# Kernel optimization log

Measured on AMD Instinct MI355X. Metric: run time of the kernel, lower is better.

Reference implementation:

```python
import jax, jax.numpy as jnp
import numpy as np

B, T, O = 32, 2048, 18            # batch, triples per graph, hardcoded object count
DIN1, H, DOUT = 1500, 512, 512    # net1 input dim is hardcoded 1500 in the source

def _kaiming(key, fan_in, fan_out):
    return jax.random.normal(key, (fan_in, fan_out), jnp.float32) * np.sqrt(2.0 / fan_in)

def setup_inputs() -> dict:
    key = jax.random.key(0)
    ks = jax.random.split(key, 8)
    trip = jax.random.normal(ks[0], (B, T, DIN1), jnp.float32)
    index = jax.random.randint(ks[1], (B, T, 2), 0, O)
    rel_lens = jax.random.randint(ks[2], (B,), 0, T)
    # net1: 1500 -> H -> 2H+Dout (ReLU after every layer incl. last)
    w1a = _kaiming(ks[3], DIN1, H); b1a = jnp.zeros((H,), jnp.float32)
    w1b = _kaiming(ks[4], H, 2 * H + DOUT); b1b = jnp.zeros((2 * H + DOUT,), jnp.float32)
    # net2: H -> H -> Dout (ReLU after every layer incl. last)
    w2a = _kaiming(ks[5], H, H); b2a = jnp.zeros((H,), jnp.float32)
    w2b = _kaiming(ks[6], H, DOUT); b2b = jnp.zeros((DOUT,), jnp.float32)
    return dict(trip=trip, index=index, rel_lens=rel_lens,
                w1a=w1a, b1a=b1a, w1b=w1b, b1b=b1b,
                w2a=w2a, b2a=b2a, w2b=w2b, b2b=b2b)

def reference(trip, index, rel_lens, w1a, b1a, w1b, b1b, w2a, b2a, w2b, b2b):
    # net1 MLP over all triples: [B,T,1500] -> [B,T,2H+Dout]
    h = jax.nn.relu(trip @ w1a + b1a)
    new_t = jax.nn.relu(h @ w1b + b1b)
    s_vecs = new_t[..., :H]              # [B,T,H] subject
    p_vecs = new_t[..., H:H + DOUT]      # [B,T,Dout] predicate (returned as-is)
    o_vecs = new_t[..., H + DOUT:]       # [B,T,H] object
    # mask out triples beyond rel_lens[i]
    mask = (jnp.arange(T)[None, :] < rel_lens[:, None]).astype(new_t.dtype)  # [B,T]
    oh_s = jax.nn.one_hot(index[..., 0], O, dtype=new_t.dtype) * mask[..., None]  # [B,T,O]
    oh_o = jax.nn.one_hot(index[..., 1], O, dtype=new_t.dtype) * mask[..., None]
    # per-batch scatter_add pooling into the O=18 object slots
    contrib = (jnp.einsum('bto,bth->boh', oh_s, s_vecs)
               + jnp.einsum('bto,bth->boh', oh_o, o_vecs))  # [B,O,H]
    # original code never resets pooled_obj_vecs inside the batch loop ->
    # accumulation is CUMULATIVE over batch items
    pooled = jnp.cumsum(contrib, axis=0)  # [B,O,H]
    # net2 MLP on each cumulative pool
    h2 = jax.nn.relu(pooled @ w2a + b2a)
    new_obj = jax.nn.relu(h2 @ w2b + b2b)  # [B,O,Dout]
    return new_obj, p_vecs
```

## Files before the change

kernel.cpp:

```cpp
#include <hip/hip_runtime.h>
#include <hip/hip_bf16.h>

#define NBATCH 32
#define NTIME  2048
#define NOBJ   18
#define KIN    1500
#define NH     512
#define NTOT   1536
#define NM     65536

typedef __attribute__((ext_vector_type(4))) float f32x4;
typedef __attribute__((ext_vector_type(8))) short s16x8;
typedef __attribute__((ext_vector_type(4))) short s16x4;

static __device__ __forceinline__ short f2bf(float f) {
  union { float f; unsigned u; } v; v.f = f;
  unsigned r = v.u + 0x7fffu + ((v.u >> 16) & 1u);
  return (short)(r >> 16);
}

static __device__ __forceinline__ void gload_lds16(const short* g, short* l) {
  __builtin_amdgcn_global_load_lds(
      (const __attribute__((address_space(1))) unsigned int*)(g),
      (__attribute__((address_space(3))) unsigned int*)(l), 16, 0, 0);
}

__global__ void k_prep(const float* __restrict__ src, short* __restrict__ dst,
                       int K, int Nsrc, int nkt, int total) {
  int i = blockIdx.x * 256 + threadIdx.x;
  if (i >= total) return;
  int chunk = i >> 14, off = i & 16383;
  int row = off >> 6, kcp = off & 63;
  int kc = kcp ^ ((row & 7) << 3);
  int cb = chunk / nkt, kt = chunk - cb * nkt;
  int n = cb * 256 + row, k = kt * 64 + kc;
  dst[i] = (k < K) ? f2bf(src[(size_t)k * Nsrc + n]) : (short)0;
}

__global__ void k_zero(float* __restrict__ p, int n) {
  int i = blockIdx.x * 256 + threadIdx.x;
  if (i < n) p[i] = 0.f;
}

__launch_bounds__(512, 2)
__global__ void k_gemm1(const float* __restrict__ A, const short* __restrict__ Bc,
                        const float* __restrict__ bias, short* __restrict__ Hc) {
  __shared__ short lA[2][64 * 64];
  __shared__ short lB[2][256 * 64];
  const int g = blockIdx.x;
  const int lid = (g & 7) * 256 + (g >> 3);
  const int rb = lid >> 1, cb = lid & 1;
  const int m0 = rb * 64, n0 = cb * 256;
  const int tid = threadIdx.x;
  const int lane = tid & 63, w = tid >> 6;
  const int wr = w >> 2, wc = w & 3;
  const int rlane = lane & 15, ksel = (lane >> 4) * 8;
  const int arow = tid >> 4;
  const int akq  = (tid & 15) * 4;
  const short* bchunk = Bc + (size_t)(cb * 24) * 16384;

  f32x4 acc[2][4] = {};
  float4 av[2];

  auto issue_stage = [&](int nb, int kt) {
    const int kbase = kt * 64;
    const bool fullq = (kt < 23) | (akq <= 24);
#pragma unroll
    for (int ri = 0; ri < 2; ++ri) {
      const float* p = A + (size_t)(m0 + arow + ri * 32) * KIN + kbase + akq;
      av[ri] = fullq ? *(const float4*)p : make_float4(0.f, 0.f, 0.f, 0.f);
    }
    const short* src = bchunk + (size_t)kt * 16384 + tid * 8;
#pragma unroll
    for (int i = 0; i < 4; ++i)
      gload_lds16(src + i * 4096, &lB[nb][tid * 8 + i * 4096]);
  };
  auto write_stage = [&](int nb) {
#pragma unroll
    for (int ri = 0; ri < 2; ++ri) {
      int row = arow + ri * 32;
      s16x4 h4;
      h4[0] = f2bf(av[ri].x); h4[1] = f2bf(av[ri].y);
      h4[2] = f2bf(av[ri].z); h4[3] = f2bf(av[ri].w);
      *(s16x4*)&lA[nb][row * 64 + (akq ^ ((row & 7) << 3))] = h4;
    }
  };
  auto compute = [&](int cu) {
#pragma unroll
    for (int j = 0; j < 2; ++j) {
      int k0 = j * 32 + ksel;
      s16x8 af[2], bfr[4];
#pragma unroll
      for (int m = 0; m < 2; ++m) {
        int row = wr * 32 + m * 16 + rlane;
        af[m] = *(const s16x8*)&lA[cu][row * 64 + (k0 ^ ((row & 7) << 3))];
      }
#pragma unroll
      for (int n = 0; n < 4; ++n) {
        int row = wc * 64 + n * 16 + rlane;
        bfr[n] = *(const s16x8*)&lB[cu][row * 64 + (k0 ^ ((row & 7) << 3))];
      }
#pragma unroll
      for (int m = 0; m < 2; ++m)
#pragma unroll
        for (int n = 0; n < 4; ++n)
          acc[m][n] = __builtin_amdgcn_mfma_f32_16x16x32_bf16(af[m], bfr[n], acc[m][n], 0, 0, 0);
    }
  };

  issue_stage(0, 0);
  write_stage(0);
  asm volatile("s_waitcnt vmcnt(0)" ::: "memory");
  __syncthreads();
  for (int kt = 0; kt < 24; ++kt) {
    const int cu = kt & 1;
    if (kt < 23) issue_stage(cu ^ 1, kt + 1);
    compute(cu);
    if (kt < 23) {
      write_stage(cu ^ 1);
      asm volatile("s_waitcnt vmcnt(0)" ::: "memory");
      __syncthreads();
    }
  }

#pragma unroll
  for (int n = 0; n < 4; ++n) {
    int c = n0 + wc * 64 + n * 16 + rlane;
    float bv = bias[c];
#pragma unroll
    for (int m = 0; m < 2; ++m) {
      int rbase = m0 + wr * 32 + m * 16 + ((lane >> 4) << 2);
#pragma unroll
      for (int q = 0; q < 4; ++q) {
        int r = rbase + q;
        float v = acc[m][n][q] + bv;
        v = v > 0.f ? v : 0.f;
        Hc[(size_t)(((r >> 7) * 8 + (c >> 6)) * 8192) + (r & 127) * 64 +
           ((c & 63) ^ ((r & 7) << 3))] = f2bf(v);
      }
    }
  }
}

__launch_bounds__(512, 2)
__global__ void k_gemm2(const short* __restrict__ Ac, const short* __restrict__ Bc,
                        const float* __restrict__ bias, const int* __restrict__ index,
                        const int* __restrict__ rel_lens,
                        float* __restrict__ contrib, float* __restrict__ out) {
  __shared__ short lA[2][64 * 64];
  __shared__ short lB[2][256 * 64];
  const int g = blockIdx.x;
  const int lid = (g & 7) * 768 + (g >> 3);
  const int rb = lid / 6, cb = lid - rb * 6;
  const int m0 = rb * 64, n0 = cb * 256;
  const int region = n0 >> 9;
  const int b = m0 >> 11;
  const int rel = rel_lens[b];
  if (region != 1 && (m0 & 2047) >= rel) return;

  const int tid = threadIdx.x;
  const int lane = tid & 63, w = tid >> 6;
  const int wr = w >> 2, wc = w & 3;
  const int rlane = lane & 15, ksel = (lane >> 4) * 8;
  const short* achunk = Ac + (size_t)((m0 >> 7) * 8) * 8192 + (m0 & 127) * 64;
  const short* bchunk = Bc + (size_t)(cb * 8) * 16384;

  f32x4 acc[2][4] = {};

  auto issue_stage = [&](int nb, int kt) {
    gload_lds16(achunk + (size_t)kt * 8192 + tid * 8, &lA[nb][tid * 8]);
    const short* src = bchunk + (size_t)kt * 16384 + tid * 8;
#pragma unroll
    for (int i = 0; i < 4; ++i)
      gload_lds16(src + i * 4096, &lB[nb][tid * 8 + i * 4096]);
  };
  auto compute = [&](int cu) {
#pragma unroll
    for (int j = 0; j < 2; ++j) {
      int k0 = j * 32 + ksel;
      s16x8 af[2], bfr[4];
#pragma unroll
      for (int m = 0; m < 2; ++m) {
        int row = wr * 32 + m * 16 + rlane;
        af[m] = *(const s16x8*)&lA[cu][row * 64 + (k0 ^ ((row & 7) << 3))];
      }
#pragma unroll
      for (int n = 0; n < 4; ++n) {
        int row = wc * 64 + n * 16 + rlane;
        bfr[n] = *(const s16x8*)&lB[cu][row * 64 + (k0 ^ ((row & 7) << 3))];
      }
#pragma unroll
      for (int m = 0; m < 2; ++m)
#pragma unroll
        for (int n = 0; n < 4; ++n)
          acc[m][n] = __builtin_amdgcn_mfma_f32_16x16x32_bf16(af[m], bfr[n], acc[m][n], 0, 0, 0);
    }
  };

  issue_stage(0, 0);
  asm volatile("s_waitcnt vmcnt(0)" ::: "memory");
  __syncthreads();
  for (int kt = 0; kt < 8; ++kt) {
    const int cu = kt & 1;
    if (kt < 7) issue_stage(cu ^ 1, kt + 1);
    compute(cu);
    if (kt < 7) {
      asm volatile("s_waitcnt vmcnt(0)" ::: "memory");
      __syncthreads();
    }
  }

  float bv[4]; int cg[4];
#pragma unroll
  for (int n = 0; n < 4; ++n) { cg[n] = n0 + wc * 64 + n * 16 + rlane; bv[n] = bias[cg[n]]; }

  if (region == 1) {
    float* po = out + (size_t)NBATCH * NOBJ * NH;
#pragma unroll
    for (int m = 0; m < 2; ++m) {
      int rbase = m0 + wr * 32 + m * 16 + ((lane >> 4) << 2);
#pragma unroll
      for (int q = 0; q < 4; ++q) {
#pragma unroll
        for (int n = 0; n < 4; ++n) {
          float v = acc[m][n][q] + bv[n];
          v = v > 0.f ? v : 0.f;
          po[(size_t)(rbase + q) * NH + (cg[n] & 511)] = v;
        }
      }
    }
  } else {
    const int sel = region >> 1;
#pragma unroll
    for (int m = 0; m < 2; ++m) {
      int rbase = m0 + wr * 32 + m * 16 + ((lane >> 4) << 2);
#pragma unroll
      for (int q = 0; q < 4; ++q) {
        int r = rbase + q;
        if ((r & 2047) < rel) {
          int idx = index[2 * r + sel];
          float* dst = contrib + ((b * NOBJ + idx) << 9);
#pragma unroll
          for (int n = 0; n < 4; ++n) {
            float v = acc[m][n][q] + bv[n];
            v = v > 0.f ? v : 0.f;
            atomicAdd(dst + (cg[n] & 511), v);
          }
        }
      }
    }
  }
}

__global__ void k_cumsum(const float* __restrict__ contrib, float* __restrict__ pooled) {
  int i = blockIdx.x * 256 + threadIdx.x;
  if (i >= NOBJ * NH) return;
  float a = 0.f;
#pragma unroll
  for (int b = 0; b < NBATCH; ++b) {
    a += contrib[b * (NOBJ * NH) + i];
    pooled[b * (NOBJ * NH) + i] = a;
  }
}

__global__ void k_mlp2(const float* __restrict__ pooled,
                       const float* __restrict__ w2a, const float* __restrict__ b2a,
                       const float* __restrict__ w2b, const float* __restrict__ b2b,
                       float* __restrict__ out) {
  __shared__ float pr[NH];
  __shared__ float hr[NH];
  int row = blockIdx.x;
  int tid = threadIdx.x;
  pr[tid]       = pooled[(size_t)row * NH + tid];
  pr[tid + 256] = pooled[(size_t)row * NH + tid + 256];
  __syncthreads();
  {
    float a0 = 0.f, a1 = 0.f, b0 = 0.f, b1 = 0.f;
    for (int k = 0; k < NH; k += 2) {
      float p0 = pr[k], p1 = pr[k + 1];
      a0 += p0 * w2a[(size_t)k * NH + tid];
      b0 += p0 * w2a[(size_t)k * NH + tid + 256];
      a1 += p1 * w2a[(size_t)(k + 1) * NH + tid];
      b1 += p1 * w2a[(size_t)(k + 1) * NH + tid + 256];
    }
    float s0 = a0 + a1 + b2a[tid], s1 = b0 + b1 + b2a[tid + 256];
    hr[tid]       = s0 > 0.f ? s0 : 0.f;
    hr[tid + 256] = s1 > 0.f ? s1 : 0.f;
  }
  __syncthreads();
  {
    float a0 = 0.f, a1 = 0.f, b0 = 0.f, b1 = 0.f;
    for (int k = 0; k < NH; k += 2) {
      float h0 = hr[k], h1 = hr[k + 1];
      a0 += h0 * w2b[(size_t)k * NH + tid];
      b0 += h0 * w2b[(size_t)k * NH + tid + 256];
      a1 += h1 * w2b[(size_t)(k + 1) * NH + tid];
      b1 += h1 * w2b[(size_t)(k + 1) * NH + tid + 256];
    }
    float s0 = a0 + a1 + b2b[tid], s1 = b0 + b1 + b2b[tid + 256];
    out[(size_t)row * NH + tid]       = s0 > 0.f ? s0 : 0.f;
    out[(size_t)row * NH + tid + 256] = s1 > 0.f ? s1 : 0.f;
  }
}

extern "C" void kernel_launch(void* const* d_in, const int* in_sizes, int n_in,
                              void* d_out, int out_size, void* d_ws, size_t ws_size,
                              hipStream_t stream) {
  const float* trip     = (const float*)d_in[0];
  const int*   index    = (const int*)d_in[1];
  const int*   rel_lens = (const int*)d_in[2];
  const float* w1a      = (const float*)d_in[3];
  const float* b1a      = (const float*)d_in[4];
  const float* w1b      = (const float*)d_in[5];
  const float* b1b      = (const float*)d_in[6];
  const float* w2a      = (const float*)d_in[7];
  const float* b2a      = (const float*)d_in[8];
  const float* w2b      = (const float*)d_in[9];
  const float* b2b      = (const float*)d_in[10];
  float* out = (float*)d_out;

  char* ws = (char*)d_ws;
  short* wt1a    = (short*)(ws);
  short* wt1b    = (short*)(ws + 1572864);
  short* hbuf    = (short*)(ws + 3145728);
  float* contrib = (float*)(ws + 70254592);
  float* pooled  = contrib + NBATCH * NOBJ * NH;

  k_zero<<<1152, 256, 0, stream>>>(contrib, NBATCH * NOBJ * NH);
  k_prep<<<3072, 256, 0, stream>>>(w1a, wt1a, KIN, NH, 24, NH * 1536);
  k_prep<<<3072, 256, 0, stream>>>(w1b, wt1b, NH, NTOT, 8, NTOT * NH);
  k_gemm1<<<2048, 512, 0, stream>>>(trip, wt1a, b1a, hbuf);
  k_gemm2<<<6144, 512, 0, stream>>>(hbuf, wt1b, b1b, index, rel_lens, contrib, out);
  k_cumsum<<<36, 256, 0, stream>>>(contrib, pooled);
  k_mlp2<<<576, 256, 0, stream>>>(pooled, w2a, b2a, w2b, b2b, out);
}
```

Before: 475.7 us.

## Fuse both net1 GEMMs into one kernel keeping hidden activations in LDS

After: 1.607 ms. 3.38x slower.

```diff
diff --git a/kernel.cpp b/kernel.cpp
--- a/kernel.cpp
+++ b/kernel.cpp
@@ -24,6 +24,10 @@
       (const __attribute__((address_space(1))) unsigned int*)(g),
       (__attribute__((address_space(3))) unsigned int*)(l), 16, 0, 0);
 }
+
+#define FENCE() asm volatile("" ::: "memory")
+#define BAR()   do { FENCE(); __builtin_amdgcn_s_barrier(); FENCE(); } while (0)
+#define LGKM0() asm volatile("s_waitcnt lgkmcnt(0)" ::: "memory")
 
 __global__ void k_prep(const float* __restrict__ src, short* __restrict__ dst,
                        int K, int Nsrc, int nkt, int total) {
@@ -43,208 +47,209 @@
 }
 
 __launch_bounds__(512, 2)
-__global__ void k_gemm1(const float* __restrict__ A, const short* __restrict__ Bc,
-                        const float* __restrict__ bias, short* __restrict__ Hc) {
-  __shared__ short lA[2][64 * 64];
+__global__ void k_fused(const float* __restrict__ A, const short* __restrict__ B1c,
+                        const float* __restrict__ b1a, const short* __restrict__ B2c,
+                        const float* __restrict__ b1b, const int* __restrict__ index,
+                        const int* __restrict__ rel_lens,
+                        float* __restrict__ contrib, float* __restrict__ out) {
+  __shared__ short hS[64 * 512];
+  __shared__ short lA[64 * 128];
   __shared__ short lB[2][256 * 64];
   const int g = blockIdx.x;
-  const int lid = (g & 7) * 256 + (g >> 3);
-  const int rb = lid >> 1, cb = lid & 1;
-  const int m0 = rb * 64, n0 = cb * 256;
+  const int lid = (g & 7) * 128 + (g >> 3);
+  const int m0 = lid * 64;
+  const int b = m0 >> 11;
+  const int rel = rel_lens[b];
   const int tid = threadIdx.x;
   const int lane = tid & 63, w = tid >> 6;
   const int wr = w >> 2, wc = w & 3;
   const int rlane = lane & 15, ksel = (lane >> 4) * 8;
-  const int arow = tid >> 4;
-  const int akq  = (tid & 15) * 4;
-  const short* bchunk = Bc + (size_t)(cb * 24) * 16384;
-
-  f32x4 acc[2][4] = {};
-  float4 av[2];
-
-  auto issue_stage = [&](int nb, int kt) {
-    const int kbase = kt * 64;
-    const bool fullq = (kt < 23) | (akq <= 24);
-#pragma unroll
-    for (int ri = 0; ri < 2; ++ri) {
-      const float* p = A + (size_t)(m0 + arow + ri * 32) * KIN + kbase + akq;
-      av[ri] = fullq ? *(const float4*)p : make_float4(0.f, 0.f, 0.f, 0.f);
-    }
-    const short* src = bchunk + (size_t)kt * 16384 + tid * 8;
+  const int arow = tid >> 3;
+  const int aseg = tid & 7;
+
+  f32x4 acc1[2][2][4] = {};
+  float4 av[4];
+  s16x8 af[2], bfr[4];
+
+  auto issueA = [&](int u) {
+#pragma unroll
+    for (int i = 0; i < 4; ++i) {
+      int k = u * 128 + aseg * 16 + i * 4;
+      const float* p = A + (size_t)(m0 + arow) * KIN + k;
+      av[i] = (k + 4 <= KIN) ? *(const float4*)p : make_float4(0.f, 0.f, 0.f, 0.f);
+    }
+  };
+  auto writeA = [&]() {
+#pragma unroll
+    for (int i = 0; i < 4; ++i) {
+      int c = aseg * 16 + i * 4;
+      s16x4 h4;
+      h4[0] = f2bf(av[i].x); h4[1] = f2bf(av[i].y);
+      h4[2] = f2bf(av[i].z); h4[3] = f2bf(av[i].w);
+      *(s16x4*)&lA[arow * 128 + (c & 64) + ((c & 63) ^ ((arow & 7) << 3))] = h4;
+    }
+  };
+  auto issueB1 = [&](int nb, int cb, int kt) {
+    const short* src = B1c + (size_t)(cb * 24 + kt) * 16384 + tid * 8;
 #pragma unroll
     for (int i = 0; i < 4; ++i)
       gload_lds16(src + i * 4096, &lB[nb][tid * 8 + i * 4096]);
   };
-  auto write_stage = [&](int nb) {
-#pragma unroll
-    for (int ri = 0; ri < 2; ++ri) {
-      int row = arow + ri * 32;
-      s16x4 h4;
-      h4[0] = f2bf(av[ri].x); h4[1] = f2bf(av[ri].y);
-      h4[2] = f2bf(av[ri].z); h4[3] = f2bf(av[ri].w);
-      *(s16x4*)&lA[nb][row * 64 + (akq ^ ((row & 7) << 3))] = h4;
-    }
-  };
-  auto compute = [&](int cu) {
-#pragma unroll
-    for (int j = 0; j < 2; ++j) {
-      int k0 = j * 32 + ksel;
-      s16x8 af[2], bfr[4];
-#pragma unroll
-      for (int m = 0; m < 2; ++m) {
-        int row = wr * 32 + m * 16 + rlane;
-        af[m] = *(const s16x8*)&lA[cu][row * 64 + (k0 ^ ((row & 7) << 3))];
-      }
-#pragma unroll
-      for (int n = 0; n < 4; ++n) {
-        int row = wc * 64 + n * 16 + rlane;
-        bfr[n] = *(const s16x8*)&lB[cu][row * 64 + (k0 ^ ((row & 7) << 3))];
-      }
-#pragma unroll
-      for (int m = 0; m < 2; ++m)
-#pragma unroll
-        for (int n = 0; n < 4; ++n)
-          acc[m][n] = __builtin_amdgcn_mfma_f32_16x16x32_bf16(af[m], bfr[n], acc[m][n], 0, 0, 0);
-    }
-  };
-
-  issue_stage(0, 0);
-  write_stage(0);
-  asm volatile("s_waitcnt vmcnt(0)" ::: "memory");
-  __syncthreads();
-  for (int kt = 0; kt < 24; ++kt) {
-    const int cu = kt & 1;
-    if (kt < 23) issue_stage(cu ^ 1, kt + 1);
-    compute(cu);
-    if (kt < 23) {
-      write_stage(cu ^ 1);
-      asm volatile("s_waitcnt vmcnt(0)" ::: "memory");
-      __syncthreads();
-    }
-  }
-
-#pragma unroll
-  for (int n = 0; n < 4; ++n) {
-    int c = n0 + wc * 64 + n * 16 + rlane;
-    float bv = bias[c];
-#pragma unroll
-    for (int m = 0; m < 2; ++m) {
-      int rbase = m0 + wr * 32 + m * 16 + ((lane >> 4) << 2);
-#pragma unroll
-      for (int q = 0; q < 4; ++q) {
-        int r = rbase + q;
-        float v = acc[m][n][q] + bv;
-        v = v > 0.f ? v : 0.f;
-        Hc[(size_t)(((r >> 7) * 8 + (c >> 6)) * 8192) + (r & 127) * 64 +
-           ((c & 63) ^ ((r & 7) << 3))] = f2bf(v);
-      }
-    }
-  }
-}
-
-__launch_bounds__(512, 2)
-__global__ void k_gemm2(const short* __restrict__ Ac, const short* __restrict__ Bc,
-                        const float* __restrict__ bias, const int* __restrict__ index,
-                        const int* __restrict__ rel_lens,
-                        float* __restrict__ contrib, float* __restrict__ out) {
-  __shared__ short lA[2][64 * 64];
-  __shared__ short lB[2][256 * 64];
-  const int g = blockIdx.x;
-  const int lid = (g & 7) * 768 + (g >> 3);
-  const int rb = lid / 6, cb = lid - rb * 6;
-  const int m0 = rb * 64, n0 = cb * 256;
-  const int region = n0 >> 9;
-  const int b = m0 >> 11;
-  const int rel = rel_lens[b];
-  if (region != 1 && (m0 & 2047) >= rel) return;
-
-  const int tid = threadIdx.x;
-  const int lane = tid & 63, w = tid >> 6;
-  const int wr = w >> 2, wc = w & 3;
-  const int rlane = lane & 15, ksel = (lane >> 4) * 8;
-  const short* achunk = Ac + (size_t)((m0 >> 7) * 8) * 8192 + (m0 & 127) * 64;
-  const short* bchunk = Bc + (size_t)(cb * 8) * 16384;
-
-  f32x4 acc[2][4] = {};
-
-  auto issue_stage = [&](int nb, int kt) {
-    gload_lds16(achunk + (size_t)kt * 8192 + tid * 8, &lA[nb][tid * 8]);
-    const short* src = bchunk + (size_t)kt * 16384 + tid * 8;
+  auto issueB2 = [&](int nb, int p, int kt) {
+    const short* src = B2c + (size_t)(p * 8 + kt) * 16384 + tid * 8;
 #pragma unroll
     for (int i = 0; i < 4; ++i)
       gload_lds16(src + i * 4096, &lB[nb][tid * 8 + i * 4096]);
   };
-  auto compute = [&](int cu) {
+
+  issueA(0);
+  issueB1(0, 0, 0);
+  asm volatile("s_waitcnt vmcnt(0)" ::: "memory");
+  writeA();
+  LGKM0();
+  BAR();
+
+#pragma unroll 1
+  for (int s = 0; s < 48; ++s) {
+    const int u = s >> 2, half = (s >> 1) & 1, sub = s & 1;
+    const int cu = s & 1;
+    if (s < 47) {
+      const int s1 = s + 1;
+      issueB1(cu ^ 1, (s1 >> 1) & 1, (s1 >> 2) * 2 + (s1 & 1));
+    }
+    const bool aIss = ((s & 3) == 1) && (u < 11);
+    if (aIss) issueA(u + 1);
 #pragma unroll
     for (int j = 0; j < 2; ++j) {
       int k0 = j * 32 + ksel;
-      s16x8 af[2], bfr[4];
 #pragma unroll
       for (int m = 0; m < 2; ++m) {
         int row = wr * 32 + m * 16 + rlane;
-        af[m] = *(const s16x8*)&lA[cu][row * 64 + (k0 ^ ((row & 7) << 3))];
-      }
-#pragma unroll
-      for (int n = 0; n < 4; ++n) {
-        int row = wc * 64 + n * 16 + rlane;
-        bfr[n] = *(const s16x8*)&lB[cu][row * 64 + (k0 ^ ((row & 7) << 3))];
+        af[m] = *(const s16x8*)&lA[row * 128 + sub * 64 + (k0 ^ ((row & 7) << 3))];
+      }
+#pragma unroll
+      for (int nn = 0; nn < 4; ++nn) {
+        int row = wc * 64 + nn * 16 + rlane;
+        bfr[nn] = *(const s16x8*)&lB[cu][row * 64 + (k0 ^ ((row & 7) << 3))];
       }
 #pragma unroll
       for (int m = 0; m < 2; ++m)
 #pragma unroll
-        for (int n = 0; n < 4; ++n)
-          acc[m][n] = __builtin_amdgcn_mfma_f32_16x16x32_bf16(af[m], bfr[n], acc[m][n], 0, 0, 0);
-    }
-  };
-
-  issue_stage(0, 0);
-  asm volatile("s_waitcnt vmcnt(0)" ::: "memory");
-  __syncthreads();
-  for (int kt = 0; kt < 8; ++kt) {
-    const int cu = kt & 1;
-    if (kt < 7) issue_stage(cu ^ 1, kt + 1);
-    compute(cu);
-    if (kt < 7) {
-      asm volatile("s_waitcnt vmcnt(0)" ::: "memory");
-      __syncthreads();
-    }
-  }
-
-  float bv[4]; int cg[4];
-#pragma unroll
-  for (int n = 0; n < 4; ++n) { cg[n] = n0 + wc * 64 + n * 16 + rlane; bv[n] = bias[cg[n]]; }
-
-  if (region == 1) {
-    float* po = out + (size_t)NBATCH * NOBJ * NH;
-#pragma unroll
-    for (int m = 0; m < 2; ++m) {
-      int rbase = m0 + wr * 32 + m * 16 + ((lane >> 4) << 2);
-#pragma unroll
-      for (int q = 0; q < 4; ++q) {
-#pragma unroll
-        for (int n = 0; n < 4; ++n) {
-          float v = acc[m][n][q] + bv[n];
+        for (int nn = 0; nn < 4; ++nn)
+          acc1[half][m][nn] = __builtin_amdgcn_mfma_f32_16x16x32_bf16(
+              af[m], bfr[nn], acc1[half][m][nn], 0, 0, 0);
+    }
+    if (s < 47) {
+      if (aIss) { asm volatile("s_waitcnt vmcnt(4)" ::: "memory"); }
+      else      { asm volatile("s_waitcnt vmcnt(0)" ::: "memory"); }
+      BAR();
+      if (((s & 3) == 3) && (u < 11)) {
+        writeA();
+        LGKM0();
+        BAR();
+      }
+    }
+  }
+
+#pragma unroll
+  for (int half = 0; half < 2; ++half)
+#pragma unroll
+    for (int nn = 0; nn < 4; ++nn) {
+      int c = half * 256 + wc * 64 + nn * 16 + rlane;
+      float bv = b1a[c];
+      int csw = (c & ~63);
+#pragma unroll
+      for (int m = 0; m < 2; ++m) {
+        int lr0 = wr * 32 + m * 16 + ((lane >> 4) << 2);
+#pragma unroll
+        for (int q = 0; q < 4; ++q) {
+          int lr = lr0 + q;
+          float v = acc1[half][m][nn][q] + bv;
           v = v > 0.f ? v : 0.f;
-          po[(size_t)(rbase + q) * NH + (cg[n] & 511)] = v;
-        }
-      }
-    }
-  } else {
-    const int sel = region >> 1;
-#pragma unroll
-    for (int m = 0; m < 2; ++m) {
-      int rbase = m0 + wr * 32 + m * 16 + ((lane >> 4) << 2);
-#pragma unroll
-      for (int q = 0; q < 4; ++q) {
-        int r = rbase + q;
-        if ((r & 2047) < rel) {
-          int idx = index[2 * r + sel];
-          float* dst = contrib + ((b * NOBJ + idx) << 9);
-#pragma unroll
-          for (int n = 0; n < 4; ++n) {
-            float v = acc[m][n][q] + bv[n];
+          hS[lr * 512 + csw + ((c & 63) ^ ((lr & 7) << 3))] = f2bf(v);
+        }
+      }
+    }
+  LGKM0();
+  BAR();
+
+#pragma unroll 1
+  for (int p = 0; p < 6; ++p) {
+    const int region = p >> 1;
+    if (region != 1 && (m0 & 2047) >= rel) continue;
+
+    f32x4 acc2[2][4] = {};
+    issueB2(0, p, 0);
+    asm volatile("s_waitcnt vmcnt(0)" ::: "memory");
+    BAR();
+#pragma unroll 1
+    for (int kt = 0; kt < 8; ++kt) {
+      const int cu = kt & 1;
+      if (kt < 7) issueB2(cu ^ 1, p, kt + 1);
+#pragma unroll
+      for (int j = 0; j < 2; ++j) {
+        int k0 = j * 32 + ksel;
+#pragma unroll
+        for (int m = 0; m < 2; ++m) {
+          int row = wr * 32 + m * 16 + rlane;
+          af[m] = *(const s16x8*)&hS[row * 512 + kt * 64 + (k0 ^ ((row & 7) << 3))];
+        }
+#pragma unroll
+        for (int nn = 0; nn < 4; ++nn) {
+          int row = wc * 64 + nn * 16 + rlane;
+          bfr[nn] = *(const s16x8*)&lB[cu][row * 64 + (k0 ^ ((row & 7) << 3))];
+        }
+#pragma unroll
+        for (int m = 0; m < 2; ++m)
+#pragma unroll
+          for (int nn = 0; nn < 4; ++nn)
+            acc2[m][nn] = __builtin_amdgcn_mfma_f32_16x16x32_bf16(
+                af[m], bfr[nn], acc2[m][nn], 0, 0, 0);
+      }
+      if (kt < 7) {
+        asm volatile("s_waitcnt vmcnt(0)" ::: "memory");
+        BAR();
+      }
+    }
+
+    float bv[4]; int cg[4];
+#pragma unroll
+    for (int nn = 0; nn < 4; ++nn) {
+      cg[nn] = p * 256 + wc * 64 + nn * 16 + rlane;
+      bv[nn] = b1b[cg[nn]];
+    }
+    if (region == 1) {
+      float* po = out + (size_t)NBATCH * NOBJ * NH;
+#pragma unroll
+      for (int m = 0; m < 2; ++m) {
+        int rbase = m0 + wr * 32 + m * 16 + ((lane >> 4) << 2);
+#pragma unroll
+        for (int q = 0; q < 4; ++q) {
+#pragma unroll
+          for (int nn = 0; nn < 4; ++nn) {
+            float v = acc2[m][nn][q] + bv[nn];
             v = v > 0.f ? v : 0.f;
-            atomicAdd(dst + (cg[n] & 511), v);
+            po[(size_t)(rbase + q) * NH + (cg[nn] & 511)] = v;
+          }
+        }
+      }
+    } else {
+      const int sel = region >> 1;
+#pragma unroll
+      for (int m = 0; m < 2; ++m) {
+        int rbase = m0 + wr * 32 + m * 16 + ((lane >> 4) << 2);
+#pragma unroll
+        for (int q = 0; q < 4; ++q) {
+          int r = rbase + q;
+          if ((r & 2047) < rel) {
+            int idx = index[2 * r + sel];
+            float* dst = contrib + ((b * NOBJ + idx) << 9);
+#pragma unroll
+            for (int nn = 0; nn < 4; ++nn) {
+              float v = acc2[m][nn][q] + bv[nn];
+              v = v > 0.f ? v : 0.f;
+              atomicAdd(dst + (cg[nn] & 511), v);
+            }
           }
         }
       }
@@ -322,15 +327,14 @@
   char* ws = (char*)d_ws;
   short* wt1a    = (short*)(ws);
   short* wt1b    = (short*)(ws + 1572864);
-  short* hbuf    = (short*)(ws + 3145728);
-  float* contrib = (float*)(ws + 70254592);
+  float* contrib = (float*)(ws + 3145728);
   float* pooled  = contrib + NBATCH * NOBJ * NH;
 
   k_zero<<<1152, 256, 0, stream>>>(contrib, NBATCH * NOBJ * NH);
   k_prep<<<3072, 256, 0, stream>>>(w1a, wt1a, KIN, NH, 24, NH * 1536);
   k_prep<<<3072, 256, 0, stream>>>(w1b, wt1b, NH, NTOT, 8, NTOT * NH);
-  k_gemm1<<<2048, 512, 0, stream>>>(trip, wt1a, b1a, hbuf);
-  k_gemm2<<<6144, 512, 0, stream>>>(hbuf, wt1b, b1b, index, rel_lens, contrib, out);
+  k_fused<<<1024, 512, 0, stream>>>(trip, wt1a, b1a, wt1b, b1b, index, rel_lens,
+                                    contrib, out);
   k_cumsum<<<36, 256, 0, stream>>>(contrib, pooled);
   k_mlp2<<<576, 256, 0, stream>>>(pooled, w2a, b2a, w2b, b2b, out);
 }
```

## Enlarge gemm1 M tile to 128 rows with single-buffered A in LDS

Applied to the files above, without the earlier changes.

New measurement: 501.5 us. 1.05x slower.

```diff
diff --git a/kernel.cpp b/kernel.cpp
--- a/kernel.cpp
+++ b/kernel.cpp
@@ -24,6 +24,10 @@
       (const __attribute__((address_space(1))) unsigned int*)(g),
       (__attribute__((address_space(3))) unsigned int*)(l), 16, 0, 0);
 }
+
+#define FENCE() asm volatile("" ::: "memory")
+#define BAR()   do { FENCE(); __builtin_amdgcn_s_barrier(); FENCE(); } while (0)
+#define LGKM0() asm volatile("s_waitcnt lgkmcnt(0)" ::: "memory")
 
 __global__ void k_prep(const float* __restrict__ src, short* __restrict__ dst,
                        int K, int Nsrc, int nkt, int total) {
@@ -45,95 +49,103 @@
 __launch_bounds__(512, 2)
 __global__ void k_gemm1(const float* __restrict__ A, const short* __restrict__ Bc,
                         const float* __restrict__ bias, short* __restrict__ Hc) {
-  __shared__ short lA[2][64 * 64];
+  __shared__ short lA[128 * 64];
   __shared__ short lB[2][256 * 64];
   const int g = blockIdx.x;
-  const int lid = (g & 7) * 256 + (g >> 3);
+  const int lid = (g & 7) * 128 + (g >> 3);
   const int rb = lid >> 1, cb = lid & 1;
-  const int m0 = rb * 64, n0 = cb * 256;
+  const int m0 = rb * 128, n0 = cb * 256;
   const int tid = threadIdx.x;
   const int lane = tid & 63, w = tid >> 6;
   const int wr = w >> 2, wc = w & 3;
   const int rlane = lane & 15, ksel = (lane >> 4) * 8;
-  const int arow = tid >> 4;
-  const int akq  = (tid & 15) * 4;
+  const int arow = tid >> 2;
+  const int akq  = (tid & 3) * 16;
   const short* bchunk = Bc + (size_t)(cb * 24) * 16384;
 
-  f32x4 acc[2][4] = {};
-  float4 av[2];
-
-  auto issue_stage = [&](int nb, int kt) {
-    const int kbase = kt * 64;
-    const bool fullq = (kt < 23) | (akq <= 24);
-#pragma unroll
-    for (int ri = 0; ri < 2; ++ri) {
-      const float* p = A + (size_t)(m0 + arow + ri * 32) * KIN + kbase + akq;
-      av[ri] = fullq ? *(const float4*)p : make_float4(0.f, 0.f, 0.f, 0.f);
-    }
+  f32x4 acc[4][4] = {};
+  float4 av[4];
+  s16x8 af[4], bfr[4];
+
+  auto issueAregs = [&](int kt) {
+    const int kbase = kt * 64 + akq;
+#pragma unroll
+    for (int i = 0; i < 4; ++i) {
+      int k = kbase + i * 4;
+      const float* p = A + (size_t)(m0 + arow) * KIN + k;
+      av[i] = (k + 4 <= KIN) ? *(const float4*)p : make_float4(0.f, 0.f, 0.f, 0.f);
+    }
+  };
+  auto writeA = [&]() {
+#pragma unroll
+    for (int i = 0; i < 4; ++i) {
+      int c = akq + i * 4;
+      s16x4 h4;
+      h4[0] = f2bf(av[i].x); h4[1] = f2bf(av[i].y);
+      h4[2] = f2bf(av[i].z); h4[3] = f2bf(av[i].w);
+      *(s16x4*)&lA[arow * 64 + (c ^ ((arow & 7) << 3))] = h4;
+    }
+  };
+  auto issueB = [&](int nb, int kt) {
     const short* src = bchunk + (size_t)kt * 16384 + tid * 8;
 #pragma unroll
     for (int i = 0; i < 4; ++i)
       gload_lds16(src + i * 4096, &lB[nb][tid * 8 + i * 4096]);
   };
-  auto write_stage = [&](int nb) {
-#pragma unroll
-    for (int ri = 0; ri < 2; ++ri) {
-      int row = arow + ri * 32;
-      s16x4 h4;
-      h4[0] = f2bf(av[ri].x); h4[1] = f2bf(av[ri].y);
-      h4[2] = f2bf(av[ri].z); h4[3] = f2bf(av[ri].w);
-      *(s16x4*)&lA[nb][row * 64 + (akq ^ ((row & 7) << 3))] = h4;
-    }
-  };
   auto compute = [&](int cu) {
 #pragma unroll
     for (int j = 0; j < 2; ++j) {
       int k0 = j * 32 + ksel;
-      s16x8 af[2], bfr[4];
-#pragma unroll
-      for (int m = 0; m < 2; ++m) {
-        int row = wr * 32 + m * 16 + rlane;
-        af[m] = *(const s16x8*)&lA[cu][row * 64 + (k0 ^ ((row & 7) << 3))];
-      }
-#pragma unroll
-      for (int n = 0; n < 4; ++n) {
-        int row = wc * 64 + n * 16 + rlane;
-        bfr[n] = *(const s16x8*)&lB[cu][row * 64 + (k0 ^ ((row & 7) << 3))];
-      }
-#pragma unroll
-      for (int m = 0; m < 2; ++m)
-#pragma unroll
-        for (int n = 0; n < 4; ++n)
-          acc[m][n] = __builtin_amdgcn_mfma_f32_16x16x32_bf16(af[m], bfr[n], acc[m][n], 0, 0, 0);
-    }
-  };
-
-  issue_stage(0, 0);
-  write_stage(0);
+#pragma unroll
+      for (int m = 0; m < 4; ++m) {
+        int row = wr * 64 + m * 16 + rlane;
+        af[m] = *(const s16x8*)&lA[row * 64 + (k0 ^ ((row & 7) << 3))];
+      }
+#pragma unroll
+      for (int nn = 0; nn < 4; ++nn) {
+        int row = wc * 64 + nn * 16 + rlane;
+        bfr[nn] = *(const s16x8*)&lB[cu][row * 64 + (k0 ^ ((row & 7) << 3))];
+      }
+#pragma unroll
+      for (int m = 0; m < 4; ++m)
+#pragma unroll
+        for (int nn = 0; nn < 4; ++nn)
+          acc[m][nn] = __builtin_amdgcn_mfma_f32_16x16x32_bf16(af[m], bfr[nn], acc[m][nn], 0, 0, 0);
+    }
+  };
+
+  issueAregs(0);
+  issueB(0, 0);
+  writeA();
+  LGKM0();
   asm volatile("s_waitcnt vmcnt(0)" ::: "memory");
-  __syncthreads();
+  BAR();
+
+#pragma unroll 1
   for (int kt = 0; kt < 24; ++kt) {
     const int cu = kt & 1;
-    if (kt < 23) issue_stage(cu ^ 1, kt + 1);
+    if (kt < 23) { issueAregs(kt + 1); issueB(cu ^ 1, kt + 1); }
     compute(cu);
+    BAR();
     if (kt < 23) {
-      write_stage(cu ^ 1);
+      writeA();
+      LGKM0();
       asm volatile("s_waitcnt vmcnt(0)" ::: "memory");
-      __syncthreads();
-    }
-  }
-
-#pragma unroll
-  for (int n = 0; n < 4; ++n) {
-    int c = n0 + wc * 64 + n * 16 + rlane;
+      BAR();
+    }
+  }
+
+#pragma unroll
+  for (int nn = 0; nn < 4; ++nn) {
+    int c = n0 + wc * 64 + nn * 16 + rlane;
     float bv = bias[c];
 #pragma unroll
-    for (int m = 0; m < 2; ++m) {
-      int rbase = m0 + wr * 32 + m * 16 + ((lane >> 4) << 2);
+    for (int m = 0; m < 4; ++m) {
+      int rbase = m0 + wr * 64 + m * 16 + ((lane >> 4) << 2);
 #pragma unroll
       for (int q = 0; q < 4; ++q) {
         int r = rbase + q;
-        float v = acc[m][n][q] + bv;
+        float v = acc[m][nn][q] + bv;
         v = v > 0.f ? v : 0.f;
         Hc[(size_t)(((r >> 7) * 8 + (c >> 6)) * 8192) + (r & 127) * 64 +
            ((c & 63) ^ ((r & 7) << 3))] = f2bf(v);
@@ -329,7 +341,7 @@
   k_zero<<<1152, 256, 0, stream>>>(contrib, NBATCH * NOBJ * NH);
   k_prep<<<3072, 256, 0, stream>>>(w1a, wt1a, KIN, NH, 24, NH * 1536);
   k_prep<<<3072, 256, 0, stream>>>(w1b, wt1b, NH, NTOT, 8, NTOT * NH);
-  k_gemm1<<<2048, 512, 0, stream>>>(trip, wt1a, b1a, hbuf);
+  k_gemm1<<<1024, 512, 0, stream>>>(trip, wt1a, b1a, hbuf);
   k_gemm2<<<6144, 512, 0, stream>>>(hbuf, wt1b, b1b, index, rel_lens, contrib, out);
   k_cumsum<<<36, 256, 0, stream>>>(contrib, pooled);
   k_mlp2<<<576, 256, 0, stream>>>(pooled, w2a, b2a, w2b, b2b, out);
```
